# Kernel optimization log

Measured on AMD Instinct MI355X. Metric: run time of the kernel, lower is better.

## Reference

```python
import jax, jax.numpy as jnp
import numpy as np

E, B, C, M, H = 8, 2, 1024, 2048, 7168


def setup_inputs() -> dict:
    key = jax.random.key(0)
    k1, k2, k3, k4 = jax.random.split(key, 4)
    # kaiming_uniform-ish scale for weights (bound = sqrt(6/fan_in)/sqrt(1+5) ~ 1/sqrt(fan_in))
    s_in = 1.0 / np.sqrt(M)
    s_ffn = 1.0 / np.sqrt(H)
    return {
        "dispatch_input": jax.random.normal(k1, (E, B, C, M), dtype=jnp.float32),
        "w1": jax.random.uniform(k2, (E, M, H), dtype=jnp.float32, minval=-s_in, maxval=s_in),
        "w2": jax.random.uniform(k3, (E, H, M), dtype=jnp.float32, minval=-s_ffn, maxval=s_ffn),
        "w3": jax.random.uniform(k4, (E, M, H), dtype=jnp.float32, minval=-s_in, maxval=s_in),
    }


def reference(dispatch_input, w1, w2, w3):
    # Batched per-expert SwiGLU MLP.
    # gate: [E,B,C,H], up: [E,B,C,H]
    gate = jnp.einsum("ebcm,emh->ebch", dispatch_input, w1)
    up = jnp.einsum("ebcm,emh->ebch", dispatch_input, w3)
    hidden = jax.nn.silu(gate) * up
    out = jnp.einsum("ebch,ehm->ebcm", hidden, w2)
    return out
```

## Files before the change

### kernel.cpp

```cpp
#include <hip/hip_runtime.h>

typedef __attribute__((ext_vector_type(8))) short bf16x8;
typedef __attribute__((ext_vector_type(4))) float f32x4;
typedef __attribute__((ext_vector_type(4))) unsigned int u32x4;
typedef __attribute__((ext_vector_type(4))) unsigned short u16x4;

#define NE 8
#define NT 2048
#define NM 2048
#define NH 7168

#define BAR() asm volatile("s_barrier" ::: "memory")
#define WAITV(N) asm volatile("s_waitcnt vmcnt(" #N ")" ::: "memory")

__device__ __forceinline__ unsigned short f2bf(float f) {
    unsigned int u = __float_as_uint(f);
    return (unsigned short)((u + 0x7fffu + ((u >> 16) & 1u)) >> 16);
}

__device__ __forceinline__ void gld16(const void* g, void* l) {
    __builtin_amdgcn_global_load_lds(
        (const __attribute__((address_space(1))) void*)g,
        (__attribute__((address_space(3))) void*)l, 16, 0, 0);
}


__global__ __launch_bounds__(256) void convert_x_kernel(
        const float* __restrict__ in, unsigned short* __restrict__ out) {
    const int i = blockIdx.x * 256 + threadIdx.x;
    f32x4 a = ((const f32x4*)in)[i];
    ((u16x4*)out)[i] = (u16x4){f2bf(a[0]), f2bf(a[1]), f2bf(a[2]), f2bf(a[3])};
}

__global__ __launch_bounds__(256) void convert_wT_kernel(
        const float* __restrict__ in, unsigned short* __restrict__ out,
        int R, int C) {
    const int t = threadIdx.x;
    const int e = blockIdx.y;
    const int tiles_c = C >> 6;
    const int tr = blockIdx.x / tiles_c, tc = blockIdx.x % tiles_c;

    const float* ip = in + (size_t)e * R * C + (size_t)(tr * 64) * C + tc * 64;
    unsigned short* op = out + (size_t)e * R * C + (size_t)(tc * 64) * R + tr * 64;

    __shared__ unsigned short tl[64][68];

    const int rr = t >> 4, c4 = (t & 15) * 4;
#pragma unroll
    for (int q = 0; q < 4; ++q) {
        const int r = q * 16 + rr;
        f32x4 v = *(const f32x4*)(ip + (size_t)r * C + c4);
        *(u16x4*)&tl[r][c4] = (u16x4){f2bf(v[0]), f2bf(v[1]), f2bf(v[2]), f2bf(v[3])};
    }
    __syncthreads();
#pragma unroll
    for (int q = 0; q < 4; ++q) {
        const int oc = q * 16 + rr;
        u16x4 v = (u16x4){tl[c4][oc], tl[c4 + 1][oc], tl[c4 + 2][oc], tl[c4 + 3][oc]};
        *(u16x4*)(op + (size_t)oc * R + c4) = v;
    }
}

__global__ __launch_bounds__(256) void convert_w13_kernel(
        const float* __restrict__ w1, const float* __restrict__ w3,
        unsigned short* __restrict__ wcat) {
    const int t = threadIdx.x;
    const int e = blockIdx.y;
    const int tiles_c = NH >> 6;
    const int tr = blockIdx.x / tiles_c, tc = blockIdx.x % tiles_c;

    __shared__ unsigned short tl[64][68];
    const int rr = t >> 4, c4 = (t & 15) * 4;
    unsigned short* ob = wcat + (size_t)e * (2 * NH) * NM + (size_t)(tc * 128) * NM + tr * 64;

#pragma unroll
    for (int pass = 0; pass < 2; ++pass) {
        const float* ip = (pass ? w3 : w1) + (size_t)e * NM * NH + (size_t)(tr * 64) * NH + tc * 64;
        if (pass) __syncthreads();
#pragma unroll
        for (int q = 0; q < 4; ++q) {
            const int r = q * 16 + rr;
            f32x4 v = *(const f32x4*)(ip + (size_t)r * NH + c4);
            *(u16x4*)&tl[r][c4] = (u16x4){f2bf(v[0]), f2bf(v[1]), f2bf(v[2]), f2bf(v[3])};
        }
        __syncthreads();
#pragma unroll
        for (int q = 0; q < 4; ++q) {
            const int oc = q * 16 + rr;
            const int orow = ((oc >> 4) * 32) + pass * 16 + (oc & 15);
            u16x4 v = (u16x4){tl[c4][oc], tl[c4 + 1][oc], tl[c4 + 2][oc], tl[c4 + 3][oc]};
            *(u16x4*)(ob + (size_t)orow * NM + c4) = v;
        }
    }
}

__global__ __launch_bounds__(512, 2) void gemm1p_kernel(
        const unsigned short* __restrict__ xb, const unsigned short* __restrict__ wcat,
        unsigned short* __restrict__ hid,
        const float* __restrict__ w2, unsigned short* __restrict__ w2t) {
    const int tid = threadIdx.x;
    const int e = blockIdx.y;
    const int d = blockIdx.x;

    __shared__ __align__(16) unsigned short lds[3 * 16384];

    if (d >= 448) {
        const int t = tid & 255;
        const int tile = (d - 448) * 2 + (tid >> 8);
        const int tr = tile >> 5, tc = tile & 31;
        const float* ip = w2 + (size_t)e * NH * NM + (size_t)(tr * 64) * NM + tc * 64;
        unsigned short* op = w2t + (size_t)e * NM * NH + (size_t)(tc * 64) * NH + tr * 64;
        unsigned short (*tl)[68] = (unsigned short (*)[68])(lds + (tid >> 8) * 4352);

        const int rr = t >> 4, c4 = (t & 15) * 4;
#pragma unroll
        for (int q = 0; q < 4; ++q) {
            const int r = q * 16 + rr;
            f32x4 v = *(const f32x4*)(ip + (size_t)r * NM + c4);
            *(u16x4*)&tl[r][c4] = (u16x4){f2bf(v[0]), f2bf(v[1]), f2bf(v[2]), f2bf(v[3])};
        }
        __syncthreads();
#pragma unroll
        for (int q = 0; q < 4; ++q) {
            const int oc = q * 16 + rr;
            u16x4 v = (u16x4){tl[c4][oc], tl[c4 + 1][oc], tl[c4 + 2][oc], tl[c4 + 3][oc]};
            *(u16x4*)(op + (size_t)oc * NH + c4) = v;
        }
        return;
    }

    const int lane = tid & 63, wv = tid >> 6;
    const int wr = wv >> 2, wc = wv & 3;
    const int l = (d & 7) * 56 + (d >> 3);
    const int ct = l >> 3, tt = l & 7;

    const unsigned short* ag = xb   + (size_t)(e * NT + tt * 256) * NM;
    const unsigned short* bg = wcat + (size_t)e * (2 * NH) * NM + (size_t)(ct * 256) * NM;
    unsigned short* hg = hid + (size_t)(e * NT + tt * 256) * NH + ct * 128;

    const int frow = lane & 15;
    const int fks  = (lane >> 4) * 8;
    const int la   = lane * 8;
    const int lr   = lane & 15, lq = lane >> 4;

    f32x4 acc[8][4];
#pragma unroll
    for (int m = 0; m < 8; ++m)
#pragma unroll
        for (int n = 0; n < 4; ++n) acc[m][n] = (f32x4){0.f, 0.f, 0.f, 0.f};

    auto stageA = [&](int t, int buf) {
        unsigned short* dst = lds + buf * 16384 + wv * 512;
        const unsigned short* src = ag + (size_t)(wv * 16 + frow) * NM + t * 32 + fks;
        gld16(src, dst);
        gld16(src + (size_t)128 * NM, dst + 8 * 512);
    };
    auto stageB = [&](int t, int buf) {
        unsigned short* dst = lds + buf * 16384 + 8192 + wv * 512;
        const unsigned short* src = bg + (size_t)(wv * 16 + frow) * NM + t * 32 + fks;
        gld16(src, dst);
        gld16(src + (size_t)128 * NM, dst + 8 * 512);
    };

    auto body = [&](int t, int buf, bool st2, int nbuf) {
        const unsigned short* bA = lds + buf * 16384;
        const unsigned short* bB = bA + 8192;
        bf16x8 af[4], bf[4];
        BAR();
#pragma unroll
        for (int m = 0; m < 4; ++m)
            af[m] = *(const bf16x8*)(bA + (wr * 8 + m) * 512 + la);
#pragma unroll
        for (int n = 0; n < 4; ++n)
            bf[n] = *(const bf16x8*)(bB + (wc * 4 + n) * 512 + la);
        __builtin_amdgcn_s_setprio(1);
#pragma unroll
        for (int m = 0; m < 4; ++m)
#pragma unroll
            for (int n = 0; n < 4; ++n)
                acc[m][n] = __builtin_amdgcn_mfma_f32_16x16x32_bf16(af[m], bf[n], acc[m][n], 0, 0, 0);
        __builtin_amdgcn_s_setprio(0);
        if (st2) stageB(t + 2, nbuf);
#pragma unroll
        for (int m = 0; m < 4; ++m)
            af[m] = *(const bf16x8*)(bA + (wr * 8 + 4 + m) * 512 + la);
        __builtin_amdgcn_s_setprio(1);
#pragma unroll
        for (int m = 0; m < 4; ++m)
#pragma unroll
            for (int n = 0; n < 4; ++n)
                acc[4 + m][n] = __builtin_amdgcn_mfma_f32_16x16x32_bf16(af[m], bf[n], acc[4 + m][n], 0, 0, 0);
        __builtin_amdgcn_s_setprio(0);
        BAR();
    };

    const int NKT = NM / 32;
    stageA(0, 0); stageB(0, 0);
    stageA(1, 1); stageB(1, 1);

    int buf = 0, nbuf = 2;
    for (int t = 0; t < NKT - 2; ++t) {
        stageA(t + 2, nbuf);
        WAITV(6);
        body(t, buf, true, nbuf);
        buf = (buf == 2) ? 0 : buf + 1;
        nbuf = (nbuf == 2) ? 0 : nbuf + 1;
    }
    WAITV(4);
    body(NKT - 2, buf, false, 0);
    buf = (buf == 2) ? 0 : buf + 1;
    WAITV(0);
    body(NKT - 1, buf, false, 0);

#pragma unroll
    for (int mf = 0; mf < 8; ++mf)
#pragma unroll
        for (int p = 0; p < 2; ++p)
#pragma unroll
            for (int i = 0; i < 4; ++i) {
                const float g = acc[mf][2 * p][i];
                const float u = acc[mf][2 * p + 1][i];
                const float s = g / (1.f + __expf(-g));
                const int r = wr * 128 + mf * 16 + lq * 4 + i;
                const int h = wc * 32 + p * 16 + lr;
                hg[(size_t)r * NH + h] = f2bf(s * u);
            }
}

__global__ __launch_bounds__(512, 2) void gemm2p_kernel(
        const unsigned short* __restrict__ hid, const unsigned short* __restrict__ w2t,
        float* __restrict__ out) {
    const int tid = threadIdx.x;
    const int lane = tid & 63, wv = tid >> 6;
    const int wr = wv >> 2, wc = wv & 3;
    const int e = blockIdx.y;
    const int d = blockIdx.x;
    const int l = (d & 7) * 8 + (d >> 3);
    const int mt = l >> 3, tt = l & 7;

    const unsigned short* ag = hid + (size_t)(e * NT + tt * 256) * NH;
    const unsigned short* bg = w2t + (size_t)e * NM * NH + (size_t)(mt * 256) * NH;
    float* og = out + (size_t)(e * NT + tt * 256) * NM + mt * 256;

    __shared__ __align__(16) unsigned short lds[3 * 16384];

    const int frow = lane & 15;
    const int fks  = (lane >> 4) * 8;
    const int la   = lane * 8;
    const int lr   = lane & 15, lq = lane >> 4;

    f32x4 acc[8][4];
#pragma unroll
    for (int m = 0; m < 8; ++m)
#pragma unroll
        for (int n = 0; n < 4; ++n) acc[m][n] = (f32x4){0.f, 0.f, 0.f, 0.f};

    auto stageA = [&](int t, int buf) {
        unsigned short* dst = lds + buf * 16384 + wv * 512;
        const unsigned short* src = ag + (size_t)(wv * 16 + frow) * NH + t * 32 + fks;
        gld16(src, dst);
        gld16(src + (size_t)128 * NH, dst + 8 * 512);
    };
    auto stageB = [&](int t, int buf) {
        unsigned short* dst = lds + buf * 16384 + 8192 + wv * 512;
        const unsigned short* src = bg + (size_t)(wv * 16 + frow) * NH + t * 32 + fks;
        gld16(src, dst);
        gld16(src + (size_t)128 * NH, dst + 8 * 512);
    };

    auto body = [&](int t, int buf, bool st2, int nbuf) {
        const unsigned short* bA = lds + buf * 16384;
        const unsigned short* bB = bA + 8192;
        bf16x8 af[4], bf[4];
        BAR();
#pragma unroll
        for (int m = 0; m < 4; ++m)
            af[m] = *(const bf16x8*)(bA + (wr * 8 + m) * 512 + la);
#pragma unroll
        for (int n = 0; n < 4; ++n)
            bf[n] = *(const bf16x8*)(bB + (wc * 4 + n) * 512 + la);
        __builtin_amdgcn_s_setprio(1);
#pragma unroll
        for (int m = 0; m < 4; ++m)
#pragma unroll
            for (int n = 0; n < 4; ++n)
                acc[m][n] = __builtin_amdgcn_mfma_f32_16x16x32_bf16(af[m], bf[n], acc[m][n], 0, 0, 0);
        __builtin_amdgcn_s_setprio(0);
        if (st2) stageB(t + 2, nbuf);
#pragma unroll
        for (int m = 0; m < 4; ++m)
            af[m] = *(const bf16x8*)(bA + (wr * 8 + 4 + m) * 512 + la);
        __builtin_amdgcn_s_setprio(1);
#pragma unroll
        for (int m = 0; m < 4; ++m)
#pragma unroll
            for (int n = 0; n < 4; ++n)
                acc[4 + m][n] = __builtin_amdgcn_mfma_f32_16x16x32_bf16(af[m], bf[n], acc[4 + m][n], 0, 0, 0);
        __builtin_amdgcn_s_setprio(0);
        BAR();
    };

    const int NKT = NH / 32;
    stageA(0, 0); stageB(0, 0);
    stageA(1, 1); stageB(1, 1);

    int buf = 0, nbuf = 2;
    for (int t = 0; t < NKT - 2; ++t) {
        stageA(t + 2, nbuf);
        WAITV(6);
        body(t, buf, true, nbuf);
        buf = (buf == 2) ? 0 : buf + 1;
        nbuf = (nbuf == 2) ? 0 : nbuf + 1;
    }
    WAITV(4);
    body(NKT - 2, buf, false, 0);
    buf = (buf == 2) ? 0 : buf + 1;
    WAITV(0);
    body(NKT - 1, buf, false, 0);

#pragma unroll
    for (int mf = 0; mf < 8; ++mf)
#pragma unroll
        for (int n = 0; n < 4; ++n)
#pragma unroll
            for (int i = 0; i < 4; ++i) {
                const int r = wr * 128 + mf * 16 + lq * 4 + i;
                const int c = wc * 64 + n * 16 + lr;
                og[(size_t)r * NM + c] = acc[mf][n][i];
            }
}

#define ROWB 80
#define TILEB (128 * ROWB)

__global__ __launch_bounds__(256, 2) void gemm1_fb_kernel(
        const float* __restrict__ x, const float* __restrict__ w1,
        const float* __restrict__ w3, unsigned short* __restrict__ hid) {
    const int tid = threadIdx.x;
    const int e = blockIdx.y;
    const int d = blockIdx.x;
    const int l = (d & 7) * 112 + (d >> 3);
    const int hn = l >> 4, tm = l & 15;

    const float* xg  = x  + (size_t)(e * NT + tm * 128) * NM;
    const float* w1g = w1 + (size_t)e * NM * NH + hn * 128;
    const float* w3g = w3 + (size_t)e * NM * NH + hn * 128;
    unsigned short* hg = hid + (size_t)(e * NT + tm * 128) * NH + hn * 128;

    __shared__ __align__(16) unsigned char lds[2 * 3 * TILEB];

    const int a_r = tid >> 3, a_c4 = tid & 7;
    const int w_kq = (tid >> 2) & 7;
    const int w_cg = ((tid >> 5) << 2) | (tid & 3);

    const int lane = tid & 63;
    const int wv = tid >> 6;
    const int r0w = (wv >> 1) * 64, c0w = (wv & 1) * 64;
    const int lr = lane & 15, lq = lane >> 4;

    f32x4 accg[4][4], accu[4][4];
#pragma unroll
    for (int m = 0; m < 4; ++m)
#pragma unroll
        for (int n = 0; n < 4; ++n) {
            accg[m][n] = (f32x4){0.f, 0.f, 0.f, 0.f};
            accu[m][n] = (f32x4){0.f, 0.f, 0.f, 0.f};
        }

    f32x4 la0, la1, la2, la3;
    f32x4 l10, l11, l12, l13, l30, l31, l32, l33;

    auto stage_load = [&](int ks) {
        const int k0 = ks * 32;
        const float* pa = xg + (size_t)a_r * NM + k0 + a_c4 * 4;
        la0 = *(const f32x4*)(pa);
        la1 = *(const f32x4*)(pa + 32 * NM);
        la2 = *(const f32x4*)(pa + 64 * NM);
        la3 = *(const f32x4*)(pa + 96 * NM);
        const float* p1 = w1g + (size_t)(k0 + w_kq * 4) * NH + w_cg * 4;
        l10 = *(const f32x4*)(p1);
        l11 = *(const f32x4*)(p1 + NH);
        l12 = *(const f32x4*)(p1 + 2 * NH);
        l13 = *(const f32x4*)(p1 + 3 * NH);
        const float* p3 = w3g + (size_t)(k0 + w_kq * 4) * NH + w_cg * 4;
        l30 = *(const f32x4*)(p3);
        l31 = *(const f32x4*)(p3 + NH);
        l32 = *(const f32x4*)(p3 + 2 * NH);
        l33 = *(const f32x4*)(p3 + 3 * NH);
    };

    auto stage_write = [&](int buf) {
        unsigned char* base = lds + buf * (3 * TILEB);
        unsigned char* pa = base + a_r * ROWB + a_c4 * 8;
        *(u16x4*)(pa)             = (u16x4){f2bf(la0[0]), f2bf(la0[1]), f2bf(la0[2]), f2bf(la0[3])};
        *(u16x4*)(pa + 32 * ROWB) = (u16x4){f2bf(la1[0]), f2bf(la1[1]), f2bf(la1[2]), f2bf(la1[3])};
        *(u16x4*)(pa + 64 * ROWB) = (u16x4){f2bf(la2[0]), f2bf(la2[1]), f2bf(la2[2]), f2bf(la2[3])};
        *(u16x4*)(pa + 96 * ROWB) = (u16x4){f2bf(la3[0]), f2bf(la3[1]), f2bf(la3[2]), f2bf(la3[3])};
        unsigned char* pw1 = base + TILEB + w_kq * 8;
#pragma unroll
        for (int j = 0; j < 4; ++j) {
            const int c = w_cg * 4 + j;
            *(u16x4*)(pw1 + c * ROWB) =
                (u16x4){f2bf(l10[j]), f2bf(l11[j]), f2bf(l12[j]), f2bf(l13[j])};
        }
        unsigned char* pw3 = base + 2 * TILEB + w_kq * 8;
#pragma unroll
        for (int j = 0; j < 4; ++j) {
            const int c = w_cg * 4 + j;
            *(u16x4*)(pw3 + c * ROWB) =
                (u16x4){f2bf(l30[j]), f2bf(l31[j]), f2bf(l32[j]), f2bf(l33[j])};
        }
    };

    auto compute = [&](int buf) {
        const unsigned char* base = lds + buf * (3 * TILEB);
        bf16x8 af[4], b1f[4], b3f[4];
#pragma unroll
        for (int m = 0; m < 4; ++m)
            af[m] = *(const bf16x8*)(base + (r0w + m * 16 + lr) * ROWB + lq * 16);
#pragma unroll
        for (int n = 0; n < 4; ++n) {
            b1f[n] = *(const bf16x8*)(base + TILEB + (c0w + n * 16 + lr) * ROWB + lq * 16);
            b3f[n] = *(const bf16x8*)(base + 2 * TILEB + (c0w + n * 16 + lr) * ROWB + lq * 16);
        }
#pragma unroll
        for (int m = 0; m < 4; ++m)
#pragma unroll
            for (int n = 0; n < 4; ++n) {
                accg[m][n] = __builtin_amdgcn_mfma_f32_16x16x32_bf16(af[m], b1f[n], accg[m][n], 0, 0, 0);
                accu[m][n] = __builtin_amdgcn_mfma_f32_16x16x32_bf16(af[m], b3f[n], accu[m][n], 0, 0, 0);
            }
    };

    stage_load(0);
    stage_write(0);
    __syncthreads();
    int cur = 0;
    const int NK = NM / 32;
    for (int ks = 0; ks < NK; ++ks) {
        const bool more = (ks + 1 < NK);
        if (more) stage_load(ks + 1);
        compute(cur);
        if (more) {
            stage_write(cur ^ 1);
            __syncthreads();
        }
        cur ^= 1;
    }

#pragma unroll
    for (int m = 0; m < 4; ++m)
#pragma unroll
        for (int n = 0; n < 4; ++n)
#pragma unroll
            for (int i = 0; i < 4; ++i) {
                const float g = accg[m][n][i];
                const float u = accu[m][n][i];
                const float s = g / (1.f + __expf(-g));
                const int r = r0w + m * 16 + lq * 4 + i;
                const int c = c0w + n * 16 + lr;
                hg[(size_t)r * NH + c] = f2bf(s * u);
            }
}

__global__ __launch_bounds__(256, 2) void gemm2_fb_kernel(
        const unsigned short* __restrict__ hid, const float* __restrict__ w2,
        float* __restrict__ out) {
    const int tid = threadIdx.x;
    const int e = blockIdx.y;
    const int d = blockIdx.x;
    const int l = (d & 7) * 32 + (d >> 3);
    const int mn = l >> 4, tm = l & 15;

    const unsigned short* ag = hid + (size_t)(e * NT + tm * 128) * NH;
    const float* wg = w2 + (size_t)e * NH * NM + mn * 128;
    float* og = out + (size_t)(e * NT + tm * 128) * NM + mn * 128;

    __shared__ __align__(16) unsigned char lds[2 * 2 * TILEB];

    const int a_row = tid >> 2, a_ch = tid & 3;
    const int w_kq = (tid >> 2) & 7;
    const int w_cg = ((tid >> 5) << 2) | (tid & 3);

    const int lane = tid & 63;
    const int wv = tid >> 6;
    const int r0w = (wv >> 1) * 64, c0w = (wv & 1) * 64;
    const int lr = lane & 15, lq = lane >> 4;

    f32x4 acc[4][4];
#pragma unroll
    for (int m = 0; m < 4; ++m)
#pragma unroll
        for (int n = 0; n < 4; ++n) acc[m][n] = (f32x4){0.f, 0.f, 0.f, 0.f};

    u32x4 lau0, lau1;
    f32x4 lw0, lw1, lw2, lw3;

    auto stage_load = [&](int ks) {
        const int k0 = ks * 32;
        lau0 = *(const u32x4*)(ag + (size_t)a_row * NH + k0 + a_ch * 8);
        lau1 = *(const u32x4*)(ag + (size_t)(a_row + 64) * NH + k0 + a_ch * 8);
        const float* p = wg + (size_t)(k0 + w_kq * 4) * NM + w_cg * 4;
        lw0 = *(const f32x4*)(p);
        lw1 = *(const f32x4*)(p + NM);
        lw2 = *(const f32x4*)(p + 2 * NM);
        lw3 = *(const f32x4*)(p + 3 * NM);
    };

    auto stage_write = [&](int buf) {
        unsigned char* base = lds + buf * (2 * TILEB);
        *(u32x4*)(base + a_row * ROWB + a_ch * 16) = lau0;
        *(u32x4*)(base + (a_row + 64) * ROWB + a_ch * 16) = lau1;
        unsigned char* pw = base + TILEB + w_kq * 8;
#pragma unroll
        for (int j = 0; j < 4; ++j) {
            const int c = w_cg * 4 + j;
            *(u16x4*)(pw + c * ROWB) =
                (u16x4){f2bf(lw0[j]), f2bf(lw1[j]), f2bf(lw2[j]), f2bf(lw3[j])};
        }
    };

    auto compute = [&](int buf) {
        const unsigned char* base = lds + buf * (2 * TILEB);
        bf16x8 af[4], bf[4];
#pragma unroll
        for (int m = 0; m < 4; ++m)
            af[m] = *(const bf16x8*)(base + (r0w + m * 16 + lr) * ROWB + lq * 16);
#pragma unroll
        for (int n = 0; n < 4; ++n)
            bf[n] = *(const bf16x8*)(base + TILEB + (c0w + n * 16 + lr) * ROWB + lq * 16);
#pragma unroll
        for (int m = 0; m < 4; ++m)
#pragma unroll
            for (int n = 0; n < 4; ++n)
                acc[m][n] = __builtin_amdgcn_mfma_f32_16x16x32_bf16(af[m], bf[n], acc[m][n], 0, 0, 0);
    };

    stage_load(0);
    stage_write(0);
    __syncthreads();
    int cur = 0;
    const int NK = NH / 32;
    for (int ks = 0; ks < NK; ++ks) {
        const bool more = (ks + 1 < NK);
        if (more) stage_load(ks + 1);
        compute(cur);
        if (more) {
            stage_write(cur ^ 1);
            __syncthreads();
        }
        cur ^= 1;
    }

#pragma unroll
    for (int m = 0; m < 4; ++m)
#pragma unroll
        for (int n = 0; n < 4; ++n)
#pragma unroll
            for (int i = 0; i < 4; ++i) {
                const int r = r0w + m * 16 + lq * 4 + i;
                const int c = c0w + n * 16 + lr;
                og[(size_t)r * NM + c] = acc[m][n][i];
            }
}


extern "C" void kernel_launch(void* const* d_in, const int* in_sizes, int n_in,
                              void* d_out, int out_size, void* d_ws, size_t ws_size,
                              hipStream_t stream) {
    const float* x  = (const float*)d_in[0];
    const float* w1 = (const float*)d_in[1];
    const float* w2 = (const float*)d_in[2];
    const float* w3 = (const float*)d_in[3];
    float* out = (float*)d_out;

    const size_t XB_SZ   = (size_t)NE * NT * NM * 2;
    const size_t WCAT_SZ = (size_t)NE * 2 * NH * NM * 2;
    const size_t HID_SZ  = (size_t)NE * NT * NH * 2;
    const size_t W2T_SZ  = (size_t)NE * NM * NH * 2;
    const size_t NEED_FULL = XB_SZ + WCAT_SZ + HID_SZ + W2T_SZ;
    const size_t NEED_STD  = XB_SZ + WCAT_SZ + HID_SZ;

    unsigned char* ws = (unsigned char*)d_ws;

    if (ws_size >= NEED_FULL) {
        unsigned short* xbp  = (unsigned short*)(ws);
        unsigned short* wcat = (unsigned short*)(ws + XB_SZ);
        unsigned short* hidb = (unsigned short*)(ws + XB_SZ + WCAT_SZ);
        unsigned short* w2t  = (unsigned short*)(ws + XB_SZ + WCAT_SZ + HID_SZ);

        convert_x_kernel<<<dim3((NE * NT * NM) / 1024), 256, 0, stream>>>(x, xbp);
        convert_w13_kernel<<<dim3((NM / 64) * (NH / 64), NE), 256, 0, stream>>>(w1, w3, wcat);
        gemm1p_kernel<<<dim3(448 + 1792, NE), 512, 0, stream>>>(xbp, wcat, hidb, w2, w2t);
        gemm2p_kernel<<<dim3(64, NE), 512, 0, stream>>>(hidb, w2t, out);
    } else if (ws_size >= NEED_STD) {
        unsigned short* xbp  = (unsigned short*)(ws);
        unsigned short* wcat = (unsigned short*)(ws + XB_SZ);
        unsigned short* hidb = (unsigned short*)(ws + XB_SZ + WCAT_SZ);
        unsigned short* w2t  = (unsigned short*)(ws);

        convert_x_kernel<<<dim3((NE * NT * NM) / 1024), 256, 0, stream>>>(x, xbp);
        convert_w13_kernel<<<dim3((NM / 64) * (NH / 64), NE), 256, 0, stream>>>(w1, w3, wcat);
        gemm1p_kernel<<<dim3(448, NE), 512, 0, stream>>>(xbp, wcat, hidb, w2, w2t);
        convert_wT_kernel<<<dim3((NH / 64) * (NM / 64), NE), 256, 0, stream>>>(w2, w2t, NH, NM);
        gemm2p_kernel<<<dim3(64, NE), 512, 0, stream>>>(hidb, w2t, out);
    } else {
        unsigned short* hid = (unsigned short*)d_ws;
        gemm1_fb_kernel<<<dim3(896, NE), 256, 0, stream>>>(x, w1, w3, hid);
        gemm2_fb_kernel<<<dim3(256, NE), 256, 0, stream>>>(hid, w2, out);
    }
}
```

Measured before the change: 1.932 ms.

## Pre-swizzle bf16 operands into fragment-contiguous tiles for GEMM staging

```diff
diff --git a/kernel.cpp b/kernel.cpp
--- a/kernel.cpp
+++ b/kernel.cpp
@@ -27,38 +27,20 @@
 
 __global__ __launch_bounds__(256) void convert_x_kernel(
         const float* __restrict__ in, unsigned short* __restrict__ out) {
-    const int i = blockIdx.x * 256 + threadIdx.x;
-    f32x4 a = ((const f32x4*)in)[i];
-    ((u16x4*)out)[i] = (u16x4){f2bf(a[0]), f2bf(a[1]), f2bf(a[2]), f2bf(a[3])};
-}
-
-__global__ __launch_bounds__(256) void convert_wT_kernel(
-        const float* __restrict__ in, unsigned short* __restrict__ out,
-        int R, int C) {
-    const int t = threadIdx.x;
-    const int e = blockIdx.y;
-    const int tiles_c = C >> 6;
-    const int tr = blockIdx.x / tiles_c, tc = blockIdx.x % tiles_c;
-
-    const float* ip = in + (size_t)e * R * C + (size_t)(tr * 64) * C + tc * 64;
-    unsigned short* op = out + (size_t)e * R * C + (size_t)(tc * 64) * R + tr * 64;
-
-    __shared__ unsigned short tl[64][68];
-
-    const int rr = t >> 4, c4 = (t & 15) * 4;
-#pragma unroll
-    for (int q = 0; q < 4; ++q) {
-        const int r = q * 16 + rr;
-        f32x4 v = *(const f32x4*)(ip + (size_t)r * C + c4);
-        *(u16x4*)&tl[r][c4] = (u16x4){f2bf(v[0]), f2bf(v[1]), f2bf(v[2]), f2bf(v[3])};
-    }
-    __syncthreads();
-#pragma unroll
-    for (int q = 0; q < 4; ++q) {
-        const int oc = q * 16 + rr;
-        u16x4 v = (u16x4){tl[c4][oc], tl[c4 + 1][oc], tl[c4 + 2][oc], tl[c4 + 3][oc]};
-        *(u16x4*)(op + (size_t)oc * R + c4) = v;
-    }
+    const int s = blockIdx.x * 256 + threadIdx.x;
+    const int l = s & 63;
+    const int f = (s >> 6) & 15;
+    const int t = (s >> 10) & 63;
+    const int tt = (s >> 16) & 7;
+    const int e = s >> 19;
+    const int tok = tt * 256 + f * 16 + (l & 15);
+    const int k = t * 32 + (l >> 4) * 8;
+    const float* p = in + (size_t)(e * NT + tok) * NM + k;
+    f32x4 a = *(const f32x4*)p;
+    f32x4 b = *(const f32x4*)(p + 4);
+    unsigned short* o = out + (size_t)s * 8;
+    *(u16x4*)o       = (u16x4){f2bf(a[0]), f2bf(a[1]), f2bf(a[2]), f2bf(a[3])};
+    *(u16x4*)(o + 4) = (u16x4){f2bf(b[0]), f2bf(b[1]), f2bf(b[2]), f2bf(b[3])};
 }
 
 __global__ __launch_bounds__(256) void convert_w13_kernel(
@@ -67,11 +49,11 @@
     const int t = threadIdx.x;
     const int e = blockIdx.y;
     const int tiles_c = NH >> 6;
-    const int tr = blockIdx.x / tiles_c, tc = blockIdx.x % tiles_c;
+    const int tr = blockIdx.x / tiles_c;
+    const int tc = blockIdx.x % tiles_c;
 
     __shared__ unsigned short tl[64][68];
     const int rr = t >> 4, c4 = (t & 15) * 4;
-    unsigned short* ob = wcat + (size_t)e * (2 * NH) * NM + (size_t)(tc * 128) * NM + tr * 64;
 
 #pragma unroll
     for (int pass = 0; pass < 2; ++pass) {
@@ -84,14 +66,55 @@
             *(u16x4*)&tl[r][c4] = (u16x4){f2bf(v[0]), f2bf(v[1]), f2bf(v[2]), f2bf(v[3])};
         }
         __syncthreads();
+        const int gk = tr * 64 + c4;
+        const int tk = gk >> 5, krun = (gk >> 3) & 3, j = gk & 7;
 #pragma unroll
         for (int q = 0; q < 4; ++q) {
             const int oc = q * 16 + rr;
-            const int orow = ((oc >> 4) * 32) + pass * 16 + (oc & 15);
+            const int gh = tc * 64 + oc;
+            const int ct = gh >> 7;
+            const int fh = (((gh >> 4) & 7) << 1) + pass;
+            const int lp = gh & 15;
             u16x4 v = (u16x4){tl[c4][oc], tl[c4 + 1][oc], tl[c4 + 2][oc], tl[c4 + 3][oc]};
-            *(u16x4*)(ob + (size_t)orow * NM + c4) = v;
-        }
-    }
+            unsigned short* dst = wcat + ((((size_t)(e * 56 + ct) * 64 + tk) * 16 + fh) << 9)
+                                  + (lp + (krun << 4)) * 8 + j;
+            *(u16x4*)dst = v;
+        }
+    }
+}
+
+__device__ __forceinline__ void w2_transpose_tile(
+        const float* __restrict__ w2, unsigned short* __restrict__ w2t,
+        int e, int tile, int t, unsigned short (*tl)[68]) {
+    const int tr = tile >> 5;
+    const int tc = tile & 31;
+    const float* ip = w2 + (size_t)e * NH * NM + (size_t)(tr * 64) * NM + tc * 64;
+    const int rr = t >> 4, c4 = (t & 15) * 4;
+#pragma unroll
+    for (int q = 0; q < 4; ++q) {
+        const int r = q * 16 + rr;
+        f32x4 v = *(const f32x4*)(ip + (size_t)r * NM + c4);
+        *(u16x4*)&tl[r][c4] = (u16x4){f2bf(v[0]), f2bf(v[1]), f2bf(v[2]), f2bf(v[3])};
+    }
+    __syncthreads();
+    const int gh = tr * 64 + c4;
+    const int tk = gh >> 5, krun = (gh >> 3) & 3, j = gh & 7;
+#pragma unroll
+    for (int q = 0; q < 4; ++q) {
+        const int oc = q * 16 + rr;
+        const int gm = tc * 64 + oc;
+        const int mt = gm >> 8, fm = (gm >> 4) & 15, lp = gm & 15;
+        u16x4 v = (u16x4){tl[c4][oc], tl[c4 + 1][oc], tl[c4 + 2][oc], tl[c4 + 3][oc]};
+        unsigned short* dst = w2t + ((((size_t)(e * 8 + mt) * 224 + tk) * 16 + fm) << 9)
+                              + (lp + (krun << 4)) * 8 + j;
+        *(u16x4*)dst = v;
+    }
+}
+
+__global__ __launch_bounds__(256) void convert_w2t_kernel(
+        const float* __restrict__ w2, unsigned short* __restrict__ w2t) {
+    __shared__ unsigned short tl[64][68];
+    w2_transpose_tile(w2, w2t, blockIdx.y, blockIdx.x, threadIdx.x, tl);
 }
 
 __global__ __launch_bounds__(512, 2) void gemm1p_kernel(
@@ -105,27 +128,9 @@
     __shared__ __align__(16) unsigned short lds[3 * 16384];
 
     if (d >= 448) {
-        const int t = tid & 255;
         const int tile = (d - 448) * 2 + (tid >> 8);
-        const int tr = tile >> 5, tc = tile & 31;
-        const float* ip = w2 + (size_t)e * NH * NM + (size_t)(tr * 64) * NM + tc * 64;
-        unsigned short* op = w2t + (size_t)e * NM * NH + (size_t)(tc * 64) * NH + tr * 64;
         unsigned short (*tl)[68] = (unsigned short (*)[68])(lds + (tid >> 8) * 4352);
-
-        const int rr = t >> 4, c4 = (t & 15) * 4;
-#pragma unroll
-        for (int q = 0; q < 4; ++q) {
-            const int r = q * 16 + rr;
-            f32x4 v = *(const f32x4*)(ip + (size_t)r * NM + c4);
-            *(u16x4*)&tl[r][c4] = (u16x4){f2bf(v[0]), f2bf(v[1]), f2bf(v[2]), f2bf(v[3])};
-        }
-        __syncthreads();
-#pragma unroll
-        for (int q = 0; q < 4; ++q) {
-            const int oc = q * 16 + rr;
-            u16x4 v = (u16x4){tl[c4][oc], tl[c4 + 1][oc], tl[c4 + 2][oc], tl[c4 + 3][oc]};
-            *(u16x4*)(op + (size_t)oc * NH + c4) = v;
-        }
+        w2_transpose_tile(w2, w2t, e, tile, tid & 255, tl);
         return;
     }
 
@@ -134,14 +139,12 @@
     const int l = (d & 7) * 56 + (d >> 3);
     const int ct = l >> 3, tt = l & 7;
 
-    const unsigned short* ag = xb   + (size_t)(e * NT + tt * 256) * NM;
-    const unsigned short* bg = wcat + (size_t)e * (2 * NH) * NM + (size_t)(ct * 256) * NM;
-    unsigned short* hg = hid + (size_t)(e * NT + tt * 256) * NH + ct * 128;
-
-    const int frow = lane & 15;
-    const int fks  = (lane >> 4) * 8;
-    const int la   = lane * 8;
-    const int lr   = lane & 15, lq = lane >> 4;
+    const unsigned short* ag = xb   + (size_t)(e * 8 + tt) * 64 * 8192;
+    const unsigned short* bg = wcat + (size_t)(e * 56 + ct) * 64 * 8192;
+    unsigned short* hb = hid + (size_t)(e * 8 + tt) * 224 * 8192;
+
+    const int la = lane * 8;
+    const int lr = lane & 15, lq = lane >> 4;
 
     f32x4 acc[8][4];
 #pragma unroll
@@ -151,15 +154,15 @@
 
     auto stageA = [&](int t, int buf) {
         unsigned short* dst = lds + buf * 16384 + wv * 512;
-        const unsigned short* src = ag + (size_t)(wv * 16 + frow) * NM + t * 32 + fks;
+        const unsigned short* src = ag + (((size_t)t * 16 + wv) << 9) + la;
         gld16(src, dst);
-        gld16(src + (size_t)128 * NM, dst + 8 * 512);
+        gld16(src + 8 * 512, dst + 8 * 512);
     };
     auto stageB = [&](int t, int buf) {
         unsigned short* dst = lds + buf * 16384 + 8192 + wv * 512;
-        const unsigned short* src = bg + (size_t)(wv * 16 + frow) * NM + t * 32 + fks;
+        const unsigned short* src = bg + (((size_t)t * 16 + wv) << 9) + la;
         gld16(src, dst);
-        gld16(src + (size_t)128 * NM, dst + 8 * 512);
+        gld16(src + 8 * 512, dst + 8 * 512);
     };
 
     auto body = [&](int t, int buf, bool st2, int nbuf) {
@@ -212,19 +215,23 @@
     WAITV(0);
     body(NKT - 1, buf, false, 0);
 
-#pragma unroll
-    for (int mf = 0; mf < 8; ++mf)
-#pragma unroll
-        for (int p = 0; p < 2; ++p)
-#pragma unroll
-            for (int i = 0; i < 4; ++i) {
-                const float g = acc[mf][2 * p][i];
-                const float u = acc[mf][2 * p + 1][i];
-                const float s = g / (1.f + __expf(-g));
-                const int r = wr * 128 + mf * 16 + lq * 4 + i;
-                const int h = wc * 32 + p * 16 + lr;
-                hg[(size_t)r * NH + h] = f2bf(s * u);
-            }
+    {
+        unsigned short* hb2 = hb + (((size_t)(ct * 4 + wc) * 16) << 9);
+        const int jj = lr & 7;
+#pragma unroll
+        for (int mf = 0; mf < 8; ++mf)
+#pragma unroll
+            for (int p = 0; p < 2; ++p)
+#pragma unroll
+                for (int i = 0; i < 4; ++i) {
+                    const float g = acc[mf][2 * p][i];
+                    const float u = acc[mf][2 * p + 1][i];
+                    const float s = g / (1.f + __expf(-g));
+                    const int fidx = wr * 8 + mf;
+                    const int lidx = (lq * 4 + i) + ((p * 2 + (lr >> 3)) << 4);
+                    hb2[((size_t)fidx << 9) + lidx * 8 + jj] = f2bf(s * u);
+                }
+    }
 }
 
 __global__ __launch_bounds__(512, 2) void gemm2p_kernel(
@@ -238,16 +245,14 @@
     const int l = (d & 7) * 8 + (d >> 3);
     const int mt = l >> 3, tt = l & 7;
 
-    const unsigned short* ag = hid + (size_t)(e * NT + tt * 256) * NH;
-    const unsigned short* bg = w2t + (size_t)e * NM * NH + (size_t)(mt * 256) * NH;
+    const unsigned short* ag = hid + (size_t)(e * 8 + tt) * 224 * 8192;
+    const unsigned short* bg = w2t + (size_t)(e * 8 + mt) * 224 * 8192;
     float* og = out + (size_t)(e * NT + tt * 256) * NM + mt * 256;
 
     __shared__ __align__(16) unsigned short lds[3 * 16384];
 
-    const int frow = lane & 15;
-    const int fks  = (lane >> 4) * 8;
-    const int la   = lane * 8;
-    const int lr   = lane & 15, lq = lane >> 4;
+    const int la = lane * 8;
+    const int lr = lane & 15, lq = lane >> 4;
 
     f32x4 acc[8][4];
 #pragma unroll
@@ -257,15 +262,15 @@
 
     auto stageA = [&](int t, int buf) {
         unsigned short* dst = lds + buf * 16384 + wv * 512;
-        const unsigned short* src = ag + (size_t)(wv * 16 + frow) * NH + t * 32 + fks;
+        const unsigned short* src = ag + (((size_t)t * 16 + wv) << 9) + la;
         gld16(src, dst);
-        gld16(src + (size_t)128 * NH, dst + 8 * 512);
+        gld16(src + 8 * 512, dst + 8 * 512);
     };
     auto stageB = [&](int t, int buf) {
         unsigned short* dst = lds + buf * 16384 + 8192 + wv * 512;
-        const unsigned short* src = bg + (size_t)(wv * 16 + frow) * NH + t * 32 + fks;
+        const unsigned short* src = bg + (((size_t)t * 16 + wv) << 9) + la;
         gld16(src, dst);
-        gld16(src + (size_t)128 * NH, dst + 8 * 512);
+        gld16(src + 8 * 512, dst + 8 * 512);
     };
 
     auto body = [&](int t, int buf, bool st2, int nbuf) {
@@ -589,7 +594,7 @@
         unsigned short* hidb = (unsigned short*)(ws + XB_SZ + WCAT_SZ);
         unsigned short* w2t  = (unsigned short*)(ws + XB_SZ + WCAT_SZ + HID_SZ);
 
-        convert_x_kernel<<<dim3((NE * NT * NM) / 1024), 256, 0, stream>>>(x, xbp);
+        convert_x_kernel<<<dim3((NE * NT * NM / 8) / 256), 256, 0, stream>>>(x, xbp);
         convert_w13_kernel<<<dim3((NM / 64) * (NH / 64), NE), 256, 0, stream>>>(w1, w3, wcat);
         gemm1p_kernel<<<dim3(448 + 1792, NE), 512, 0, stream>>>(xbp, wcat, hidb, w2, w2t);
         gemm2p_kernel<<<dim3(64, NE), 512, 0, stream>>>(hidb, w2t, out);
@@ -599,10 +604,10 @@
         unsigned short* hidb = (unsigned short*)(ws + XB_SZ + WCAT_SZ);
         unsigned short* w2t  = (unsigned short*)(ws);
 
-        convert_x_kernel<<<dim3((NE * NT * NM) / 1024), 256, 0, stream>>>(x, xbp);
+        convert_x_kernel<<<dim3((NE * NT * NM / 8) / 256), 256, 0, stream>>>(x, xbp);
         convert_w13_kernel<<<dim3((NM / 64) * (NH / 64), NE), 256, 0, stream>>>(w1, w3, wcat);
         gemm1p_kernel<<<dim3(448, NE), 512, 0, stream>>>(xbp, wcat, hidb, w2, w2t);
-        convert_wT_kernel<<<dim3((NH / 64) * (NM / 64), NE), 256, 0, stream>>>(w2, w2t, NH, NM);
+        convert_w2t_kernel<<<dim3((NH / 64) * (NM / 64), NE), 256, 0, stream>>>(w2, w2t);
         gemm2p_kernel<<<dim3(64, NE), 512, 0, stream>>>(hidb, w2t, out);
     } else {
         unsigned short* hid = (unsigned short*)d_ws;
```

Result: faster. 1.658 ms (-14.2%).
